# Optimization experiments

Hardware: AMD Instinct MI355X
Metric: run time of the kernel (lower is better)

The kernel has to match this reference:

```python
import jax, jax.numpy as jnp
import numpy as np

N_NODES = 10000
N_EDGES = 160000
IN_CH = 1030
HID = 256
HEADS = 4
OUT_CH = 49
NEG_SLOPE = 0.2
EPS = 1e-5


def setup_inputs() -> dict:
    key = jax.random.key(0)
    ks = jax.random.split(key, 20)
    HC = HID * HEADS  # 1024
    inp = {
        "x": jax.random.normal(ks[0], (N_NODES, IN_CH), dtype=jnp.float32),
        "edge_index": jax.random.randint(ks[1], (2, N_EDGES), 0, N_NODES, dtype=jnp.int64),
        # conv1 (GATv2): lin_l (source), lin_r (target), att, out bias
        "c1_wl": jax.random.normal(ks[2], (IN_CH, HC), dtype=jnp.float32) * 0.03,
        "c1_bl": jnp.zeros((HC,), dtype=jnp.float32),
        "c1_wr": jax.random.normal(ks[3], (IN_CH, HC), dtype=jnp.float32) * 0.03,
        "c1_br": jnp.zeros((HC,), dtype=jnp.float32),
        "c1_att": jax.random.normal(ks[4], (HEADS, HID), dtype=jnp.float32) * 0.06,
        "c1_bias": jnp.zeros((HC,), dtype=jnp.float32),
        # norm1 (per-node LayerNorm over channels)
        "ln1_w": jnp.ones((HC,), dtype=jnp.float32),
        "ln1_b": jnp.zeros((HC,), dtype=jnp.float32),
        # conv2
        "c2_wl": jax.random.normal(ks[5], (HC, HC), dtype=jnp.float32) * 0.03,
        "c2_bl": jnp.zeros((HC,), dtype=jnp.float32),
        "c2_wr": jax.random.normal(ks[6], (HC, HC), dtype=jnp.float32) * 0.03,
        "c2_br": jnp.zeros((HC,), dtype=jnp.float32),
        "c2_att": jax.random.normal(ks[7], (HEADS, HID), dtype=jnp.float32) * 0.06,
        "c2_bias": jnp.zeros((HC,), dtype=jnp.float32),
        # norm2
        "ln2_w": jnp.ones((HC,), dtype=jnp.float32),
        "ln2_b": jnp.zeros((HC,), dtype=jnp.float32),
        # classifier: Linear(HC, HID) -> ELU -> Linear(HID, OUT_CH)
        "cls_w1": jax.random.normal(ks[8], (HC, HID), dtype=jnp.float32) * 0.03,
        "cls_b1": jnp.zeros((HID,), dtype=jnp.float32),
        "cls_w2": jax.random.normal(ks[9], (HID, OUT_CH), dtype=jnp.float32) * 0.06,
        "cls_b2": jnp.zeros((OUT_CH,), dtype=jnp.float32),
    }
    return inp


def gatv2_conv(x, src, dst, wl, bl, wr, br, att, bias, n_nodes):
    """PyG GATv2Conv, concat heads. src/dst include self loops."""
    H, C = att.shape
    xl = (x @ wl + bl).reshape(-1, H, C)  # source transform [N,H,C]
    xr = (x @ wr + br).reshape(-1, H, C)  # target transform [N,H,C]
    m = xl[src] + xr[dst]                  # [E,H,C] gather + add
    e = jnp.einsum("ehc,hc->eh", jax.nn.leaky_relu(m, NEG_SLOPE), att)  # [E,H]
    # segment softmax over destination node
    emax = jax.ops.segment_max(e, dst, num_segments=n_nodes)
    p = jnp.exp(e - emax[dst])
    denom = jax.ops.segment_sum(p, dst, num_segments=n_nodes)
    alpha = p / (denom[dst] + 1e-16)       # [E,H]
    out = jax.ops.segment_sum(xl[src] * alpha[:, :, None], dst, num_segments=n_nodes)
    return out.reshape(n_nodes, H * C) + bias


def layer_norm(x, w, b):
    mu = jnp.mean(x, axis=-1, keepdims=True)
    var = jnp.var(x, axis=-1, keepdims=True)
    return (x - mu) / jnp.sqrt(var + EPS) * w + b


def reference(x, edge_index, c1_wl, c1_bl, c1_wr, c1_br, c1_att, c1_bias,
              ln1_w, ln1_b, c2_wl, c2_bl, c2_wr, c2_br, c2_att, c2_bias,
              ln2_w, ln2_b, cls_w1, cls_b1, cls_w2, cls_b2):
    n = x.shape[0]
    loops = jnp.arange(n, dtype=edge_index.dtype)
    src = jnp.concatenate([edge_index[0], loops])  # add_self_loops=True
    dst = jnp.concatenate([edge_index[1], loops])

    h = gatv2_conv(x, src, dst, c1_wl, c1_bl, c1_wr, c1_br, c1_att, c1_bias, n)
    h = jax.nn.elu(layer_norm(h, ln1_w, ln1_b))
    # dropout: identity at inference
    h = gatv2_conv(h, src, dst, c2_wl, c2_bl, c2_wr, c2_br, c2_att, c2_bias, n)
    h = jax.nn.elu(layer_norm(h, ln2_w, ln2_b))
    h = jax.nn.elu(h @ cls_w1 + cls_b1)
    return h @ cls_w2 + cls_b2  # [N, 49]
```

## Files before the change

### kernel.cpp

```cpp
#include <hip/hip_runtime.h>
#include <stdint.h>

#define N_NODES 10000
#define N_EDGES 160000
#define E_TOT   170000
#define IN_CH   1030
#define HC      1024
#define OUT_CH  49
#define NEG_SLOPE 0.2f
#define LN_EPS 1e-5f
#define LOG2E 1.4426950408889634f

#define MPAD  10112
#define K1PAD 1088

typedef __attribute__((ext_vector_type(8))) __bf16 bf16x8;
typedef __attribute__((ext_vector_type(4))) float floatx4;
typedef __attribute__((ext_vector_type(2))) float floatx2;
typedef _Float16 h2 __attribute__((ext_vector_type(2)));

static __device__ __forceinline__ unsigned short f2bf(float f) {
  union { float f; uint32_t u; } v; v.f = f;
  uint32_t u = v.u;
  u += 0x7fffu + ((u >> 16) & 1u);
  return (unsigned short)(u >> 16);
}
static __device__ __forceinline__ unsigned short f2h(float f) {
  _Float16 h = (_Float16)f;
  union { _Float16 h; unsigned short u; } v; v.h = h; return v.u;
}
static __device__ __forceinline__ h2 bits2h2(uint32_t u) {
  union { uint32_t i; h2 h; } v; v.i = u; return v.h;
}
static __device__ __forceinline__ floatx2 h2f2(h2 a) {
  floatx2 r; r.x = (float)a.x; r.y = (float)a.y; return r;
}

static __device__ __forceinline__ float wred_add(float x) {
#define DPP_ADD(ctrl, rmask)                                                   \
  x += __builtin_bit_cast(float, __builtin_amdgcn_update_dpp(                  \
           0, __builtin_bit_cast(int, x), ctrl, rmask, 0xf, true))
  DPP_ADD(0x111, 0xf);
  DPP_ADD(0x112, 0xf);
  DPP_ADD(0x114, 0xf);
  DPP_ADD(0x118, 0xf);
  DPP_ADD(0x142, 0xa);
  DPP_ADD(0x143, 0xc);
#undef DPP_ADD
  return __builtin_bit_cast(float,
      __builtin_amdgcn_readlane(__builtin_bit_cast(int, x), 63));
}


__global__ void cast_x_kernel(const float* __restrict__ x, unsigned short* __restrict__ xa,
                              int* __restrict__ counts) {
  int idx = blockIdx.x * 256 + threadIdx.x;
  if (idx < N_NODES) counts[idx] = 0;
  if (idx >= N_NODES * K1PAD) return;
  int m = idx / K1PAD, k = idx - m * K1PAD;
  float v = (k < IN_CH) ? x[m * IN_CH + k] : 0.f;
  xa[idx] = f2bf(v);
}

static __device__ __forceinline__ void transpose_body(
    float (*tile)[33], const float* __restrict__ wa, const float* __restrict__ wb,
    int split, int lda, int ldb, int Kvalid, int Kout,
    unsigned short* __restrict__ out, int bx, int by, int t) {
  int n0 = bx * 32, k0 = by * 32;
  int tx = t & 31, ty = t >> 5;
#pragma unroll
  for (int i = 0; i < 4; i++) {
    int k = k0 + ty + i * 8;
    int n = n0 + tx;
    float v = 0.f;
    if (k < Kvalid) v = (n < split) ? wa[(size_t)k * lda + n] : wb[(size_t)k * ldb + (n - split)];
    tile[ty + i * 8][tx] = v;
  }
  __syncthreads();
#pragma unroll
  for (int i = 0; i < 4; i++) {
    int n = n0 + ty + i * 8;
    int k = k0 + tx;
    out[(size_t)n * Kout + k] = f2bf(tile[tx][ty + i * 8]);
  }
}

#define NB_W1 2176
#define NB_W2 2048
#define NB_WC 256
#define NB_CNT 665
__global__ __launch_bounds__(256) void prep2_kernel(
    const float* __restrict__ c1_wl, const float* __restrict__ c1_wr,
    const float* __restrict__ c2_wl, const float* __restrict__ c2_wr,
    const float* __restrict__ cls_w1,
    const int* __restrict__ dstArr, int* __restrict__ counts,
    unsigned short* __restrict__ wt1, unsigned short* __restrict__ wt2,
    unsigned short* __restrict__ wtc1)
{
  __shared__ float tile[32][33];
  int b = blockIdx.x, t = threadIdx.x;
  if (b < NB_W1) {
    transpose_body(tile, c1_wl, c1_wr, 1024, 1024, 1024, IN_CH, K1PAD, wt1, b & 63, b >> 6, t);
  } else if (b < NB_W1 + NB_W2) {
    int bb = b - NB_W1;
    transpose_body(tile, c2_wl, c2_wr, 1024, 1024, 1024, 1024, 1024, wt2, bb & 63, bb >> 6, t);
  } else if (b < NB_W1 + NB_W2 + NB_WC) {
    int bb = b - (NB_W1 + NB_W2);
    transpose_body(tile, cls_w1, cls_w1, 256, 256, 256, 1024, 1024, wtc1, bb & 7, bb >> 3, t);
  } else {
    int e = (b - (NB_W1 + NB_W2 + NB_WC)) * 256 + t;
    if (e < E_TOT) {
      int d = (e < N_EDGES) ? dstArr[e] : (e - N_EDGES);
      atomicAdd(&counts[d], 1);
    }
  }
}

__global__ __launch_bounds__(256) void scan_kernel(const int* __restrict__ counts,
                                                   int* __restrict__ rstart,
                                                   int* __restrict__ rwork) {
  __shared__ int sm[256];
  int t = threadIdx.x;
  int b0 = t * 40;
  int b1 = b0 + 40; if (b1 > N_NODES) b1 = N_NODES; if (b0 > N_NODES) b0 = N_NODES;
  int s = 0;
  for (int i = b0; i < b1; i++) s += counts[i];
  sm[t] = s; __syncthreads();
  for (int st = 1; st < 256; st <<= 1) {
    int add = (t >= st) ? sm[t - st] : 0;
    __syncthreads();
    sm[t] += add;
    __syncthreads();
  }
  int run = sm[t] - s;
  for (int i = b0; i < b1; i++) { rstart[i] = run; rwork[i] = run; run += counts[i]; }
  if (t == 255) rstart[N_NODES] = run;
}

__global__ void scatter_kernel(const int* __restrict__ srcArr, const int* __restrict__ dstArr,
                               int* __restrict__ rwork, int* __restrict__ csrsrc) {
  int e = blockIdx.x * 256 + threadIdx.x;
  if (e >= E_TOT) return;
  int d, sv;
  if (e < N_EDGES) { d = dstArr[e]; sv = srcArr[e]; }
  else { d = e - N_EDGES; sv = d; }
  int pos = atomicAdd(&rwork[d], 1);
  csrsrc[pos] = sv;
}

template <int MODE, int KC>
__global__ __launch_bounds__(256, 4) void gemm_bf16(
    const unsigned short* __restrict__ A, const unsigned short* __restrict__ Bt,
    float* __restrict__ Cf, unsigned short* __restrict__ Cb,
    const float* __restrict__ blo, const float* __restrict__ bhi,
    int M, int ldc, int bsplit)
{
  __shared__ __align__(16) unsigned short As[128 * 64];
  __shared__ __align__(16) unsigned short Bs[128 * 64];
  const int t = threadIdx.x;
  const int w = t >> 6, lane = t & 63;

  const unsigned int nwg = gridDim.x * gridDim.y;
  const unsigned int bid = blockIdx.y * gridDim.x + blockIdx.x;
  const unsigned int q8 = nwg >> 3, r8 = nwg & 7;
  const unsigned int xcd = bid & 7, sub = bid >> 3;
  const unsigned int wg = (xcd < r8 ? xcd * (q8 + 1) : r8 * (q8 + 1) + (xcd - r8) * q8) + sub;
  const int tile_n = (wg % gridDim.x) * 128, tile_m = (wg / gridDim.x) * 128;

  floatx4 acc[4][4] = {};

  const int qq = w * 64 + lane;
  const int row0 = qq >> 3;
  const int gj = (qq & 7) ^ (row0 & 7);
  const unsigned short* gA0 = A  + (size_t)(tile_m + row0) * KC + gj * 8;
  const unsigned short* gB0 = Bt + (size_t)(tile_n + row0) * KC + gj * 8;

  const int wm = (w >> 1) * 64, wn = (w & 1) * 64;
  const int lrow = lane & 15, cg0 = (lane >> 4);
  const int sw = lrow & 7;

#pragma unroll 1
  for (int k0 = 0; k0 < KC; k0 += 64) {
#pragma unroll
    for (int p = 0; p < 4; p++) {
      __builtin_amdgcn_global_load_lds(
          (const __attribute__((address_space(1))) void*)(gA0 + p * 32 * KC),
          (__attribute__((address_space(3))) void*)(As + p * 2048 + w * 512), 16, 0, 0);
      __builtin_amdgcn_global_load_lds(
          (const __attribute__((address_space(1))) void*)(gB0 + p * 32 * KC),
          (__attribute__((address_space(3))) void*)(Bs + p * 2048 + w * 512), 16, 0, 0);
    }
    gA0 += 64; gB0 += 64;
    __syncthreads();
#pragma unroll
    for (int h = 0; h < 2; h++) {
      const int sc = (h * 4 + cg0) ^ sw;
      bf16x8 a[4], b[4];
#pragma unroll
      for (int mi = 0; mi < 4; mi++)
        a[mi] = *(const bf16x8*)(As + (wm + mi * 16 + lrow) * 64 + sc * 8);
#pragma unroll
      for (int ni = 0; ni < 4; ni++)
        b[ni] = *(const bf16x8*)(Bs + (wn + ni * 16 + lrow) * 64 + sc * 8);
#pragma unroll
      for (int mi = 0; mi < 4; mi++)
#pragma unroll
        for (int ni = 0; ni < 4; ni++)
          acc[mi][ni] = __builtin_amdgcn_mfma_f32_16x16x32_bf16(a[mi], b[ni], acc[mi][ni], 0, 0, 0);
    }
    __syncthreads();
  }

  const int rbase = (lane >> 4) * 4;
#pragma unroll
  for (int mi = 0; mi < 4; mi++) {
#pragma unroll
    for (int r = 0; r < 4; r++) {
      int m = tile_m + wm + mi * 16 + rbase + r;
      if (m >= M) continue;
#pragma unroll
      for (int ni = 0; ni < 4; ni++) {
        int n = tile_n + wn + ni * 16 + lrow;
        float v = acc[mi][ni][r] + (n < bsplit ? blo[n] : bhi[n - bsplit]);
        if (MODE == 0) {
          Cf[(size_t)m * ldc + n] = v;
        } else if (MODE == 1) {
          Cf[(size_t)m * ldc + n] = v > 0.f ? v : expm1f(v);
        } else {
          Cb[(size_t)m * 2048 + n] = f2h(v);
        }
      }
    }
  }
}


__global__ __launch_bounds__(256) void gat_ln_kernel(
    const unsigned short* __restrict__ xlr,
    const float* __restrict__ att,
    const int* __restrict__ csrsrc, const int* __restrict__ rstart,
    const float* __restrict__ bias,
    const float* __restrict__ lnw, const float* __restrict__ lnb,
    unsigned short* __restrict__ out)
{
  const int d = blockIdx.x;
  const int t = threadIdx.x;
  const int lane = t & 63, wv = t >> 6;
  const int c = wv * 256 + lane * 4;

  uint2 xru = *(const uint2*)(xlr + (size_t)d * 2048 + 1024 + c);
  h2 xr0 = bits2h2(xru.x), xr1 = bits2h2(xru.y);
  float4 aw4 = *(const float4*)(att + c);
  h2 aw0, aw1;
  aw0.x = (_Float16)(aw4.x * LOG2E); aw0.y = (_Float16)(aw4.y * LOG2E);
  aw1.x = (_Float16)(aw4.z * LOG2E); aw1.y = (_Float16)(aw4.w * LOG2E);
  const h2 ns = {(_Float16)NEG_SLOPE, (_Float16)NEG_SLOPE};
  const unsigned short* xbase = xlr + c;

  const int start = rstart[d], end = rstart[d + 1];
  const int last = end - 1;
  const int ngroups = (end - start + 3) >> 2;

  float m = -3.0e38f, l = 0.f;
  floatx2 accA = {0.f, 0.f}, accB = {0.f, 0.f};

#define CIDX(e) csrsrc[(e) < last ? (e) : last]
  int sA0 = CIDX(start),     sA1 = CIDX(start + 1);
  int sA2 = CIDX(start + 2), sA3 = CIDX(start + 3);
  uint2 uA0 = *(const uint2*)(xbase + (size_t)sA0 * 2048);
  uint2 uA1 = *(const uint2*)(xbase + (size_t)sA1 * 2048);
  uint2 uA2 = *(const uint2*)(xbase + (size_t)sA2 * 2048);
  uint2 uA3 = *(const uint2*)(xbase + (size_t)sA3 * 2048);
  int sB0 = CIDX(start + 4), sB1 = CIDX(start + 5);
  int sB2 = CIDX(start + 6), sB3 = CIDX(start + 7);

  for (int g = 0; g < ngroups; g++) {
    const int base = start + (g << 2);
    int sC0 = CIDX(base + 8),  sC1 = CIDX(base + 9);
    int sC2 = CIDX(base + 10), sC3 = CIDX(base + 11);
    uint2 uB0 = *(const uint2*)(xbase + (size_t)sB0 * 2048);
    uint2 uB1 = *(const uint2*)(xbase + (size_t)sB1 * 2048);
    uint2 uB2 = *(const uint2*)(xbase + (size_t)sB2 * 2048);
    uint2 uB3 = *(const uint2*)(xbase + (size_t)sB3 * 2048);

    h2 xh0a = bits2h2(uA0.x), xh0b = bits2h2(uA0.y);
    h2 xh1a = bits2h2(uA1.x), xh1b = bits2h2(uA1.y);
    h2 xh2a = bits2h2(uA2.x), xh2b = bits2h2(uA2.y);
    h2 xh3a = bits2h2(uA3.x), xh3b = bits2h2(uA3.y);
    h2 t0a = xh0a + xr0, t0b = xh0b + xr1;
    h2 t1a = xh1a + xr0, t1b = xh1b + xr1;
    h2 t2a = xh2a + xr0, t2b = xh2b + xr1;
    h2 t3a = xh3a + xr0, t3b = xh3b + xr1;
    h2 r0a = __builtin_elementwise_max(t0a, t0a * ns);
    h2 r0b = __builtin_elementwise_max(t0b, t0b * ns);
    h2 r1a = __builtin_elementwise_max(t1a, t1a * ns);
    h2 r1b = __builtin_elementwise_max(t1b, t1b * ns);
    h2 r2a = __builtin_elementwise_max(t2a, t2a * ns);
    h2 r2b = __builtin_elementwise_max(t2b, t2b * ns);
    h2 r3a = __builtin_elementwise_max(t3a, t3a * ns);
    h2 r3b = __builtin_elementwise_max(t3b, t3b * ns);
    float p0 = __builtin_amdgcn_fdot2(r0b, aw1, __builtin_amdgcn_fdot2(r0a, aw0, 0.f, false), false);
    float p1 = __builtin_amdgcn_fdot2(r1b, aw1, __builtin_amdgcn_fdot2(r1a, aw0, 0.f, false), false);
    float p2 = __builtin_amdgcn_fdot2(r2b, aw1, __builtin_amdgcn_fdot2(r2a, aw0, 0.f, false), false);
    float p3 = __builtin_amdgcn_fdot2(r3b, aw1, __builtin_amdgcn_fdot2(r3a, aw0, 0.f, false), false);
    p0 = wred_add(p0);
    p1 = wred_add(p1);
    p2 = wred_add(p2);
    p3 = wred_add(p3);
    float mx = fmaxf(fmaxf(p0, p1), fmaxf(p2, p3));
    if (mx > m) {
      float sc = exp2f(m - mx);
      floatx2 scv; scv.x = sc; scv.y = sc;
      accA *= scv; accB *= scv; l *= sc;
      m = mx;
    }
    float pe0 = exp2f(p0 - m);
    float pe1 = (base + 1 <= last) ? exp2f(p1 - m) : 0.f;
    float pe2 = (base + 2 <= last) ? exp2f(p2 - m) : 0.f;
    float pe3 = (base + 3 <= last) ? exp2f(p3 - m) : 0.f;
    floatx2 x0A = h2f2(xh0a), x0B = h2f2(xh0b);
    floatx2 x1A = h2f2(xh1a), x1B = h2f2(xh1b);
    floatx2 x2A = h2f2(xh2a), x2B = h2f2(xh2b);
    floatx2 x3A = h2f2(xh3a), x3B = h2f2(xh3b);
    floatx2 v0; v0.x = pe0; v0.y = pe0;
    floatx2 v1; v1.x = pe1; v1.y = pe1;
    floatx2 v2; v2.x = pe2; v2.y = pe2;
    floatx2 v3; v3.x = pe3; v3.y = pe3;
    accA += x0A * v0; accA += x1A * v1; accA += x2A * v2; accA += x3A * v3;
    accB += x0B * v0; accB += x1B * v1; accB += x2B * v2; accB += x3B * v3;
    l += pe0 + pe1 + pe2 + pe3;

    uA0 = uB0; uA1 = uB1; uA2 = uB2; uA3 = uB3;
    sB0 = sC0; sB1 = sC1; sB2 = sC2; sB3 = sC3;
  }
#undef CIDX

  float rd = 1.f / (l + 1e-16f);
  float4 bv = *(const float4*)(bias + c);
  float o0 = accA.x * rd + bv.x, o1 = accA.y * rd + bv.y;
  float o2 = accB.x * rd + bv.z, o3 = accB.y * rd + bv.w;

  __shared__ float ws1[4], ws2[4];
  float s1 = o0 + o1 + o2 + o3;
  float s2 = o0 * o0 + o1 * o1 + o2 * o2 + o3 * o3;
#pragma unroll
  for (int mm = 32; mm >= 1; mm >>= 1) {
    s1 += __shfl_xor(s1, mm, 64);
    s2 += __shfl_xor(s2, mm, 64);
  }
  if (lane == 0) { ws1[wv] = s1; ws2[wv] = s2; }
  __syncthreads();
  float mean = (ws1[0] + ws1[1] + ws1[2] + ws1[3]) * (1.f / 1024.f);
  float var  = (ws2[0] + ws2[1] + ws2[2] + ws2[3]) * (1.f / 1024.f) - mean * mean;
  float rstd = rsqrtf(var + LN_EPS);
  float4 wv4 = *(const float4*)(lnw + c);
  float4 bb  = *(const float4*)(lnb + c);
  float z0 = (o0 - mean) * rstd * wv4.x + bb.x; z0 = z0 > 0.f ? z0 : expm1f(z0);
  float z1 = (o1 - mean) * rstd * wv4.y + bb.y; z1 = z1 > 0.f ? z1 : expm1f(z1);
  float z2 = (o2 - mean) * rstd * wv4.z + bb.z; z2 = z2 > 0.f ? z2 : expm1f(z2);
  float z3 = (o3 - mean) * rstd * wv4.w + bb.w; z3 = z3 > 0.f ? z3 : expm1f(z3);
  ushort4 u;
  u.x = f2bf(z0); u.y = f2bf(z1); u.z = f2bf(z2); u.w = f2bf(z3);
  *(ushort4*)(out + (size_t)d * 1024 + c) = u;
}


__global__ __launch_bounds__(64) void cls2_kernel(
    const float* __restrict__ h3, const float* __restrict__ w2,
    const float* __restrict__ b2, float* __restrict__ out)
{
  __shared__ float row[256];
  int node = blockIdx.x, t = threadIdx.x;
  *(float4*)(row + t * 4) = *(const float4*)(h3 + (size_t)node * 256 + t * 4);
  __syncthreads();
  if (t < OUT_CH) {
    float a0 = 0.f, a1 = 0.f, a2 = 0.f, a3 = 0.f;
#pragma unroll 4
    for (int k = 0; k < 256; k += 4) {
      float4 r = *(const float4*)(row + k);
      a0 += r.x * w2[(k + 0) * OUT_CH + t];
      a1 += r.y * w2[(k + 1) * OUT_CH + t];
      a2 += r.z * w2[(k + 2) * OUT_CH + t];
      a3 += r.w * w2[(k + 3) * OUT_CH + t];
    }
    out[node * OUT_CH + t] = (a0 + a1) + (a2 + a3) + b2[t];
  }
}


extern "C" void kernel_launch(void* const* d_in, const int* in_sizes, int n_in,
                              void* d_out, int out_size, void* d_ws, size_t ws_size,
                              hipStream_t stream)
{
  const float* x       = (const float*)d_in[0];
  const int*   ei      = (const int*)d_in[1];
  const float* c1_wl   = (const float*)d_in[2];
  const float* c1_bl   = (const float*)d_in[3];
  const float* c1_wr   = (const float*)d_in[4];
  const float* c1_br   = (const float*)d_in[5];
  const float* c1_att  = (const float*)d_in[6];
  const float* c1_bias = (const float*)d_in[7];
  const float* ln1_w   = (const float*)d_in[8];
  const float* ln1_b   = (const float*)d_in[9];
  const float* c2_wl   = (const float*)d_in[10];
  const float* c2_bl   = (const float*)d_in[11];
  const float* c2_wr   = (const float*)d_in[12];
  const float* c2_br   = (const float*)d_in[13];
  const float* c2_att  = (const float*)d_in[14];
  const float* c2_bias = (const float*)d_in[15];
  const float* ln2_w   = (const float*)d_in[16];
  const float* ln2_b   = (const float*)d_in[17];
  const float* cls_w1  = (const float*)d_in[18];
  const float* cls_b1  = (const float*)d_in[19];
  const float* cls_w2  = (const float*)d_in[20];
  const float* cls_b2  = (const float*)d_in[21];

  const int* srcArr = ei;
  const int* dstArr = ei + N_EDGES;

  char* ws = (char*)d_ws;
  size_t off = 0;
  auto alloc = [&](size_t bytes) { void* p = ws + off; off += (bytes + 255) & ~(size_t)255; return p; };
  unsigned short* xa      = (unsigned short*)alloc((size_t)MPAD * K1PAD * 2);
  unsigned short* wt1     = (unsigned short*)alloc((size_t)2048 * K1PAD * 2);
  unsigned short* wt2     = (unsigned short*)alloc((size_t)2048 * 1024 * 2);
  unsigned short* wtc1    = (unsigned short*)alloc((size_t)256 * 1024 * 2);
  unsigned short* xlr     = (unsigned short*)alloc((size_t)N_NODES * 2048 * 2);
  float*          h3      = (float*)alloc((size_t)N_NODES * 256 * 4);
  unsigned short* hb      = (unsigned short*)alloc((size_t)MPAD * 1024 * 2);
  int*            counts  = (int*)alloc(N_NODES * 4);
  int*            rwork   = (int*)alloc(N_NODES * 4);
  int*            rstart  = (int*)alloc((N_NODES + 1) * 4);
  int*            csrsrc  = (int*)alloc(E_TOT * 4);
  (void)in_sizes; (void)n_in; (void)out_size; (void)ws_size;

  cast_x_kernel<<<(N_NODES * K1PAD + 255) / 256, 256, 0, stream>>>(x, xa, counts);
  prep2_kernel<<<NB_W1 + NB_W2 + NB_WC + NB_CNT, 256, 0, stream>>>(
      c1_wl, c1_wr, c2_wl, c2_wr, cls_w1, dstArr, counts, wt1, wt2, wtc1);

  scan_kernel<<<1, 256, 0, stream>>>(counts, rstart, rwork);
  scatter_kernel<<<(E_TOT + 255) / 256, 256, 0, stream>>>(srcArr, dstArr, rwork, csrsrc);

  gemm_bf16<2, K1PAD><<<dim3(16, 79), 256, 0, stream>>>(xa, wt1, nullptr, xlr, c1_bl, c1_br, N_NODES, 0, 1024);
  gat_ln_kernel<<<N_NODES, 256, 0, stream>>>(xlr, c1_att, csrsrc, rstart, c1_bias, ln1_w, ln1_b, hb);

  gemm_bf16<2, 1024><<<dim3(16, 79), 256, 0, stream>>>(hb, wt2, nullptr, xlr, c2_bl, c2_br, N_NODES, 0, 1024);
  gat_ln_kernel<<<N_NODES, 256, 0, stream>>>(xlr, c2_att, csrsrc, rstart, c2_bias, ln2_w, ln2_b, hb);

  gemm_bf16<1, 1024><<<dim3(2, 79), 256, 0, stream>>>(hb, wtc1, h3, nullptr, cls_b1, cls_b1, N_NODES, 256, 1024);
  cls2_kernel<<<N_NODES, 64, 0, stream>>>(h3, cls_w2, cls_b2, (float*)d_out);
}
```

Measured before the change: 498.3 us.

## Split GAT edge loop into exact quad body and scalar tail, batch classifier nodes

The attention aggregation loop now runs full groups of four edges with no per-edge validity checks or clamped indices, then handles leftover edges one at a time. This removes the wasted duplicate loads and exp work on padded edges and simplifies index arithmetic. The CSR array is padded by 16 zeroed entries so lookahead prefetches stay in bounds. Separately, the GEMM epilogue hoists per-column bias loads out of the row loop, and the final classifier packs four nodes per 256-thread block instead of one node per 64-thread block.

```diff
diff --git a/kernel.cpp b/kernel.cpp
--- a/kernel.cpp
+++ b/kernel.cpp
@@ -141,6 +141,7 @@
                                int* __restrict__ rwork, int* __restrict__ csrsrc) {
   int e = blockIdx.x * 256 + threadIdx.x;
   if (e >= E_TOT) return;
+  if (e < 16) csrsrc[E_TOT + e] = 0;
   int d, sv;
   if (e < N_EDGES) { d = dstArr[e]; sv = srcArr[e]; }
   else { d = e - N_EDGES; sv = d; }
@@ -211,6 +212,13 @@
     __syncthreads();
   }
 
+  float bcol[4];
+#pragma unroll
+  for (int ni = 0; ni < 4; ni++) {
+    int n = tile_n + wn + ni * 16 + lrow;
+    bcol[ni] = (n < bsplit) ? blo[n] : bhi[n - bsplit];
+  }
+
   const int rbase = (lane >> 4) * 4;
 #pragma unroll
   for (int mi = 0; mi < 4; mi++) {
@@ -221,7 +229,7 @@
 #pragma unroll
       for (int ni = 0; ni < 4; ni++) {
         int n = tile_n + wn + ni * 16 + lrow;
-        float v = acc[mi][ni][r] + (n < bsplit ? blo[n] : bhi[n - bsplit]);
+        float v = acc[mi][ni][r] + bcol[ni];
         if (MODE == 0) {
           Cf[(size_t)m * ldc + n] = v;
         } else if (MODE == 1) {
@@ -257,83 +265,100 @@
   const h2 ns = {(_Float16)NEG_SLOPE, (_Float16)NEG_SLOPE};
   const unsigned short* xbase = xlr + c;
 
-  const int start = rstart[d], end = rstart[d + 1];
-  const int last = end - 1;
-  const int ngroups = (end - start + 3) >> 2;
+  int start = rstart[d], deg = rstart[d + 1] - start;
 
   float m = -3.0e38f, l = 0.f;
   floatx2 accA = {0.f, 0.f}, accB = {0.f, 0.f};
 
-#define CIDX(e) csrsrc[(e) < last ? (e) : last]
-  int sA0 = CIDX(start),     sA1 = CIDX(start + 1);
-  int sA2 = CIDX(start + 2), sA3 = CIDX(start + 3);
-  uint2 uA0 = *(const uint2*)(xbase + (size_t)sA0 * 2048);
-  uint2 uA1 = *(const uint2*)(xbase + (size_t)sA1 * 2048);
-  uint2 uA2 = *(const uint2*)(xbase + (size_t)sA2 * 2048);
-  uint2 uA3 = *(const uint2*)(xbase + (size_t)sA3 * 2048);
-  int sB0 = CIDX(start + 4), sB1 = CIDX(start + 5);
-  int sB2 = CIDX(start + 6), sB3 = CIDX(start + 7);
-
-  for (int g = 0; g < ngroups; g++) {
-    const int base = start + (g << 2);
-    int sC0 = CIDX(base + 8),  sC1 = CIDX(base + 9);
-    int sC2 = CIDX(base + 10), sC3 = CIDX(base + 11);
-    uint2 uB0 = *(const uint2*)(xbase + (size_t)sB0 * 2048);
-    uint2 uB1 = *(const uint2*)(xbase + (size_t)sB1 * 2048);
-    uint2 uB2 = *(const uint2*)(xbase + (size_t)sB2 * 2048);
-    uint2 uB3 = *(const uint2*)(xbase + (size_t)sB3 * 2048);
-
-    h2 xh0a = bits2h2(uA0.x), xh0b = bits2h2(uA0.y);
-    h2 xh1a = bits2h2(uA1.x), xh1b = bits2h2(uA1.y);
-    h2 xh2a = bits2h2(uA2.x), xh2b = bits2h2(uA2.y);
-    h2 xh3a = bits2h2(uA3.x), xh3b = bits2h2(uA3.y);
+  int i = 0;
+  if (deg >= 4) {
+    int sA0 = csrsrc[start],     sA1 = csrsrc[start + 1];
+    int sA2 = csrsrc[start + 2], sA3 = csrsrc[start + 3];
+    uint2 uA0 = *(const uint2*)(xbase + (size_t)sA0 * 2048);
+    uint2 uA1 = *(const uint2*)(xbase + (size_t)sA1 * 2048);
+    uint2 uA2 = *(const uint2*)(xbase + (size_t)sA2 * 2048);
+    uint2 uA3 = *(const uint2*)(xbase + (size_t)sA3 * 2048);
+    int sB0 = csrsrc[start + 4], sB1 = csrsrc[start + 5];
+    int sB2 = csrsrc[start + 6], sB3 = csrsrc[start + 7];
+    for (; i + 4 <= deg; i += 4) {
+      int sC0 = csrsrc[start + i + 8],  sC1 = csrsrc[start + i + 9];
+      int sC2 = csrsrc[start + i + 10], sC3 = csrsrc[start + i + 11];
+      uint2 uB0 = *(const uint2*)(xbase + (size_t)sB0 * 2048);
+      uint2 uB1 = *(const uint2*)(xbase + (size_t)sB1 * 2048);
+      uint2 uB2 = *(const uint2*)(xbase + (size_t)sB2 * 2048);
+      uint2 uB3 = *(const uint2*)(xbase + (size_t)sB3 * 2048);
+
+      h2 xh0a = bits2h2(uA0.x), xh0b = bits2h2(uA0.y);
+      h2 xh1a = bits2h2(uA1.x), xh1b = bits2h2(uA1.y);
+      h2 xh2a = bits2h2(uA2.x), xh2b = bits2h2(uA2.y);
+      h2 xh3a = bits2h2(uA3.x), xh3b = bits2h2(uA3.y);
+      h2 t0a = xh0a + xr0, t0b = xh0b + xr1;
+      h2 t1a = xh1a + xr0, t1b = xh1b + xr1;
+      h2 t2a = xh2a + xr0, t2b = xh2b + xr1;
+      h2 t3a = xh3a + xr0, t3b = xh3b + xr1;
+      h2 r0a = __builtin_elementwise_max(t0a, t0a * ns);
+      h2 r0b = __builtin_elementwise_max(t0b, t0b * ns);
+      h2 r1a = __builtin_elementwise_max(t1a, t1a * ns);
+      h2 r1b = __builtin_elementwise_max(t1b, t1b * ns);
+      h2 r2a = __builtin_elementwise_max(t2a, t2a * ns);
+      h2 r2b = __builtin_elementwise_max(t2b, t2b * ns);
+      h2 r3a = __builtin_elementwise_max(t3a, t3a * ns);
+      h2 r3b = __builtin_elementwise_max(t3b, t3b * ns);
+      float p0 = __builtin_amdgcn_fdot2(r0b, aw1, __builtin_amdgcn_fdot2(r0a, aw0, 0.f, false), false);
+      float p1 = __builtin_amdgcn_fdot2(r1b, aw1, __builtin_amdgcn_fdot2(r1a, aw0, 0.f, false), false);
+      float p2 = __builtin_amdgcn_fdot2(r2b, aw1, __builtin_amdgcn_fdot2(r2a, aw0, 0.f, false), false);
+      float p3 = __builtin_amdgcn_fdot2(r3b, aw1, __builtin_amdgcn_fdot2(r3a, aw0, 0.f, false), false);
+      p0 = wred_add(p0);
+      p1 = wred_add(p1);
+      p2 = wred_add(p2);
+      p3 = wred_add(p3);
+      float mx = fmaxf(fmaxf(p0, p1), fmaxf(p2, p3));
+      if (mx > m) {
+        float sc = exp2f(m - mx);
+        floatx2 scv; scv.x = sc; scv.y = sc;
+        accA *= scv; accB *= scv; l *= sc;
+        m = mx;
+      }
+      float pe0 = exp2f(p0 - m), pe1 = exp2f(p1 - m);
+      float pe2 = exp2f(p2 - m), pe3 = exp2f(p3 - m);
+      floatx2 x0A = h2f2(xh0a), x0B = h2f2(xh0b);
+      floatx2 x1A = h2f2(xh1a), x1B = h2f2(xh1b);
+      floatx2 x2A = h2f2(xh2a), x2B = h2f2(xh2b);
+      floatx2 x3A = h2f2(xh3a), x3B = h2f2(xh3b);
+      floatx2 v0; v0.x = pe0; v0.y = pe0;
+      floatx2 v1; v1.x = pe1; v1.y = pe1;
+      floatx2 v2; v2.x = pe2; v2.y = pe2;
+      floatx2 v3; v3.x = pe3; v3.y = pe3;
+      accA += x0A * v0; accA += x1A * v1; accA += x2A * v2; accA += x3A * v3;
+      accB += x0B * v0; accB += x1B * v1; accB += x2B * v2; accB += x3B * v3;
+      l += pe0 + pe1 + pe2 + pe3;
+
+      uA0 = uB0; uA1 = uB1; uA2 = uB2; uA3 = uB3;
+      sB0 = sC0; sB1 = sC1; sB2 = sC2; sB3 = sC3;
+    }
+  }
+  for (; i < deg; i++) {
+    int s0 = csrsrc[start + i];
+    uint2 u0 = *(const uint2*)(xbase + (size_t)s0 * 2048);
+    h2 xh0a = bits2h2(u0.x), xh0b = bits2h2(u0.y);
     h2 t0a = xh0a + xr0, t0b = xh0b + xr1;
-    h2 t1a = xh1a + xr0, t1b = xh1b + xr1;
-    h2 t2a = xh2a + xr0, t2b = xh2b + xr1;
-    h2 t3a = xh3a + xr0, t3b = xh3b + xr1;
     h2 r0a = __builtin_elementwise_max(t0a, t0a * ns);
     h2 r0b = __builtin_elementwise_max(t0b, t0b * ns);
-    h2 r1a = __builtin_elementwise_max(t1a, t1a * ns);
-    h2 r1b = __builtin_elementwise_max(t1b, t1b * ns);
-    h2 r2a = __builtin_elementwise_max(t2a, t2a * ns);
-    h2 r2b = __builtin_elementwise_max(t2b, t2b * ns);
-    h2 r3a = __builtin_elementwise_max(t3a, t3a * ns);
-    h2 r3b = __builtin_elementwise_max(t3b, t3b * ns);
     float p0 = __builtin_amdgcn_fdot2(r0b, aw1, __builtin_amdgcn_fdot2(r0a, aw0, 0.f, false), false);
-    float p1 = __builtin_amdgcn_fdot2(r1b, aw1, __builtin_amdgcn_fdot2(r1a, aw0, 0.f, false), false);
-    float p2 = __builtin_amdgcn_fdot2(r2b, aw1, __builtin_amdgcn_fdot2(r2a, aw0, 0.f, false), false);
-    float p3 = __builtin_amdgcn_fdot2(r3b, aw1, __builtin_amdgcn_fdot2(r3a, aw0, 0.f, false), false);
     p0 = wred_add(p0);
-    p1 = wred_add(p1);
-    p2 = wred_add(p2);
-    p3 = wred_add(p3);
-    float mx = fmaxf(fmaxf(p0, p1), fmaxf(p2, p3));
-    if (mx > m) {
-      float sc = exp2f(m - mx);
+    if (p0 > m) {
+      float sc = exp2f(m - p0);
       floatx2 scv; scv.x = sc; scv.y = sc;
       accA *= scv; accB *= scv; l *= sc;
-      m = mx;
+      m = p0;
     }
     float pe0 = exp2f(p0 - m);
-    float pe1 = (base + 1 <= last) ? exp2f(p1 - m) : 0.f;
-    float pe2 = (base + 2 <= last) ? exp2f(p2 - m) : 0.f;
-    float pe3 = (base + 3 <= last) ? exp2f(p3 - m) : 0.f;
     floatx2 x0A = h2f2(xh0a), x0B = h2f2(xh0b);
-    floatx2 x1A = h2f2(xh1a), x1B = h2f2(xh1b);
-    floatx2 x2A = h2f2(xh2a), x2B = h2f2(xh2b);
-    floatx2 x3A = h2f2(xh3a), x3B = h2f2(xh3b);
-    floatx2 v0; v0.x = pe0; v0.y = pe0;
-    floatx2 v1; v1.x = pe1; v1.y = pe1;
-    floatx2 v2; v2.x = pe2; v2.y = pe2;
-    floatx2 v3; v3.x = pe3; v3.y = pe3;
-    accA += x0A * v0; accA += x1A * v1; accA += x2A * v2; accA += x3A * v3;
-    accB += x0B * v0; accB += x1B * v1; accB += x2B * v2; accB += x3B * v3;
-    l += pe0 + pe1 + pe2 + pe3;
-
-    uA0 = uB0; uA1 = uB1; uA2 = uB2; uA3 = uB3;
-    sB0 = sC0; sB1 = sC1; sB2 = sC2; sB3 = sC3;
-  }
-#undef CIDX
+    floatx2 pe0v; pe0v.x = pe0; pe0v.y = pe0;
+    accA += x0A * pe0v;
+    accB += x0B * pe0v;
+    l += pe0;
+  }
 
   float rd = 1.f / (l + 1e-16f);
   float4 bv = *(const float4*)(bias + c);
@@ -365,25 +390,25 @@
 }
 
 
-__global__ __launch_bounds__(64) void cls2_kernel(
+__global__ __launch_bounds__(256) void cls2_kernel(
     const float* __restrict__ h3, const float* __restrict__ w2,
     const float* __restrict__ b2, float* __restrict__ out)
 {
-  __shared__ float row[256];
-  int node = blockIdx.x, t = threadIdx.x;
-  *(float4*)(row + t * 4) = *(const float4*)(h3 + (size_t)node * 256 + t * 4);
+  __shared__ float row[4][256];
+  int t = threadIdx.x, wv = t >> 6, lane = t & 63;
+  int node = blockIdx.x * 4 + wv;
+  *(float4*)(&row[wv][lane * 4]) = *(const float4*)(h3 + (size_t)node * 256 + lane * 4);
   __syncthreads();
-  if (t < OUT_CH) {
+  if (lane < OUT_CH) {
     float a0 = 0.f, a1 = 0.f, a2 = 0.f, a3 = 0.f;
 #pragma unroll 4
     for (int k = 0; k < 256; k += 4) {
-      float4 r = *(const float4*)(row + k);
-      a0 += r.x * w2[(k + 0) * OUT_CH + t];
-      a1 += r.y * w2[(k + 1) * OUT_CH + t];
-      a2 += r.z * w2[(k + 2) * OUT_CH + t];
-      a3 += r.w * w2[(k + 3) * OUT_CH + t];
-    }
-    out[node * OUT_CH + t] = (a0 + a1) + (a2 + a3) + b2[t];
+      a0 += row[wv][k]     * w2[(k    ) * OUT_CH + lane];
+      a1 += row[wv][k + 1] * w2[(k + 1) * OUT_CH + lane];
+      a2 += row[wv][k + 2] * w2[(k + 2) * OUT_CH + lane];
+      a3 += row[wv][k + 3] * w2[(k + 3) * OUT_CH + lane];
+    }
+    out[node * OUT_CH + lane] = (a0 + a1) + (a2 + a3) + b2[lane];
   }
 }
 
@@ -431,7 +456,7 @@
   int*            counts  = (int*)alloc(N_NODES * 4);
   int*            rwork   = (int*)alloc(N_NODES * 4);
   int*            rstart  = (int*)alloc((N_NODES + 1) * 4);
-  int*            csrsrc  = (int*)alloc(E_TOT * 4);
+  int*            csrsrc  = (int*)alloc((E_TOT + 16) * 4);
   (void)in_sizes; (void)n_in; (void)out_size; (void)ws_size;
 
   cast_x_kernel<<<(N_NODES * K1PAD + 255) / 256, 256, 0, stream>>>(x, xa, counts);
@@ -448,5 +473,5 @@
   gat_ln_kernel<<<N_NODES, 256, 0, stream>>>(xlr, c2_att, csrsrc, rstart, c2_bias, ln2_w, ln2_b, hb);
 
   gemm_bf16<1, 1024><<<dim3(2, 79), 256, 0, stream>>>(hb, wtc1, h3, nullptr, cls_b1, cls_b1, N_NODES, 256, 1024);
-  cls2_kernel<<<N_NODES, 64, 0, stream>>>(h3, cls_w2, cls_b2, (float*)d_out);
-}
+  cls2_kernel<<<2500, 256, 0, stream>>>(h3, cls_w2, cls_b2, (float*)d_out);
+}
```

New measurement: 458.6 us. 8.0% less time.
